# Optimization experiments

Measured on AMD Instinct MI355X. Metric: run time of the kernel, lower is better.

The kernel has to match this reference:

```python
import jax, jax.numpy as jnp
import numpy as np
from jax import lax

B, C, H, W = 8, 512, 48, 48
E = 512          # embed_dim (== in_channels, required by GLoR fusion channel math)
P = 128          # ContextBlock planes = int(512*0.25)
NC = 2           # num_classes; also used (buggily, but faithfully) as BGAM threshold
TOPK_RATIO = 0.1


def conv1x1(x, w, b=None):
    # w: [out, in]
    y = jnp.einsum('bchw,oc->bohw', x, w)
    if b is not None:
        y = y + b[None, :, None, None]
    return y


def conv3x3(x, w, b):
    y = lax.conv_general_dilated(x, w, (1, 1), 'SAME',
                                 dimension_numbers=('NCHW', 'OIHW', 'NCHW'))
    return y + b[None, :, None, None]


def dwconv3x3(x, w):
    # depthwise: w [C,1,3,3], feature_group_count=C
    return lax.conv_general_dilated(x, w, (1, 1), 'SAME',
                                    dimension_numbers=('NCHW', 'OIHW', 'NCHW'),
                                    feature_group_count=x.shape[1])


def bn_eval(x, g, b):
    # eval-mode BatchNorm2d, running_mean=0, running_var=1, eps=1e-5
    scale = g / jnp.sqrt(1.0 + 1e-5)
    return x * scale[None, :, None, None] + b[None, :, None, None]


def chan_mlp(c, w1, b1, g, bl, w2, b2):
    # ContextBlock channel transform: 1x1 conv -> LayerNorm([P,1,1]) -> ReLU -> 1x1 conv, on [B,C] vectors
    h = c @ w1.T + b1                                  # [B,P]
    mu = h.mean(-1, keepdims=True)
    var = jnp.var(h, axis=-1, keepdims=True)
    h = (h - mu) / jnp.sqrt(var + 1e-5) * g + bl
    h = jax.nn.relu(h)
    return h @ w2.T + b2                               # [B,C]


def cos_self(t):
    # torch F.cosine_similarity(t, t, dim=1): dot/(max(n,eps)*max(n,eps)), eps=1e-8
    nrm2 = jnp.sum(t * t, axis=1)                      # [B,H,W]
    n = jnp.maximum(jnp.sqrt(nrm2), 1e-8)
    return nrm2 / (n * n)


def setup_inputs() -> dict:
    key = jax.random.key(0)
    ks = iter(jax.random.split(key, 64))
    def nrm(shape, scale):
        return (jax.random.normal(next(ks), shape) * scale).astype(jnp.float32)
    def gma(n):
        return (1.0 + 0.05 * jax.random.normal(next(ks), (n,))).astype(jnp.float32)
    def bta(n):
        return (0.05 * jax.random.normal(next(ks), (n,))).astype(jnp.float32)
    sC = 1.0 / np.sqrt(C)
    return dict(
        x=jax.random.normal(next(ks), (B, C, H, W), jnp.float32),
        # GLoR local ConvBranch
        lb_w1=nrm((E, C), sC), lb_g1=gma(E), lb_b1=bta(E),
        lb_w2=nrm((E, 1, 3, 3), 1.0 / 3.0), lb_g2=gma(E), lb_b2=bta(E),
        lb_w3=nrm((E, E), 1.0 / np.sqrt(E)), lb_g3=gma(E), lb_b3=bta(E),
        # GLoR ContextBlock (att pooling, channel_add + channel_mul)
        cm_w=nrm((1, C), sC), cm_b=bta(1),
        ca_w1=nrm((P, C), sC), ca_b1=bta(P), ca_lg=gma(P), ca_lb=bta(P),
        ca_w2=nrm((C, P), 1.0 / np.sqrt(P)), ca_b2=bta(C),
        cmu_w1=nrm((P, C), sC), cmu_b1=bta(P), cmu_lg=gma(P), cmu_lb=bta(P),
        cmu_w2=nrm((C, P), 1.0 / np.sqrt(P)), cmu_b2=bta(C),
        fu_w=nrm((E, 2 * E), 1.0 / np.sqrt(2 * E)), fu_b=bta(E),
        # heads
        sh_w=nrm((NC, E), 1.0 / np.sqrt(E)), sh_b=bta(NC),
        bh_w=nrm((2, E), 1.0 / np.sqrt(E)), bh_b=bta(2),
        # ReverseAttention
        ra_w1=nrm((2, 2, 3, 3), 1.0 / np.sqrt(18)), ra_b1=bta(2), ra_g1=gma(2), ra_bb1=bta(2),
        ra_w2=nrm((2, 2, 3, 3), 1.0 / np.sqrt(18)), ra_b2=bta(2), ra_g2=gma(2), ra_bb2=bta(2),
        # AGCR (all bias=False)
        q_w=nrm((E // 4, E), 1.0 / np.sqrt(E)), k_w=nrm((E // 4, E), 1.0 / np.sqrt(E)),
        v_w=nrm((E, E), 1.0 / np.sqrt(E)), fin_w=nrm((E, 2 * E), 1.0 / np.sqrt(2 * E)),
    )


def reference(x, lb_w1, lb_g1, lb_b1, lb_w2, lb_g2, lb_b2, lb_w3, lb_g3, lb_b3,
              cm_w, cm_b, ca_w1, ca_b1, ca_lg, ca_lb, ca_w2, ca_b2,
              cmu_w1, cmu_b1, cmu_lg, cmu_lb, cmu_w2, cmu_b2, fu_w, fu_b,
              sh_w, sh_b, bh_w, bh_b,
              ra_w1, ra_b1, ra_g1, ra_bb1, ra_w2, ra_b2, ra_g2, ra_bb2,
              q_w, k_w, v_w, fin_w):
    b_, c_, h_, w_ = x.shape
    N = h_ * w_
    # ---- GLoR: local ConvBranch ----
    t = jax.nn.relu(bn_eval(conv1x1(x, lb_w1), lb_g1, lb_b1))
    t = jax.nn.relu(bn_eval(dwconv3x3(t, lb_w2), lb_g2, lb_b2))
    local = bn_eval(conv1x1(t, lb_w3), lb_g3, lb_b3)
    # ---- GLoR: ContextBlock (att pooling) ----
    xf = x.reshape(b_, c_, N)
    mask = (conv1x1(x, cm_w, cm_b)).reshape(b_, 1, N)
    mask = jax.nn.softmax(mask, axis=2)
    ctx = jnp.einsum('bcn,bn->bc', xf, mask[:, 0, :])              # [B,C]
    mul = jax.nn.sigmoid(chan_mlp(ctx, cmu_w1, cmu_b1, cmu_lg, cmu_lb, cmu_w2, cmu_b2))
    add = chan_mlp(ctx, ca_w1, ca_b1, ca_lg, ca_lb, ca_w2, ca_b2)
    glob = x * mul[:, :, None, None] + add[:, :, None, None]
    gx = conv1x1(jnp.concatenate([local, glob], axis=1), fu_w, fu_b)  # [B,E,H,W]
    # ---- heads ----
    sem = conv1x1(gx, sh_w, sh_b)                                   # [B,NC,H,W]
    bdl = conv1x1(gx, bh_w, bh_b)                                   # [B,2,H,W]
    # ---- ReverseAttention(boundary_logits, sigmoid(boundary_logits)) ----
    wx = bdl * (1.0 - jax.nn.sigmoid(bdl))
    r = jax.nn.relu(bn_eval(conv3x3(wx, ra_w1, ra_b1), ra_g1, ra_bb1))
    r = jax.nn.relu(bn_eval(conv3x3(r, ra_w2, ra_b2), ra_g2, ra_bb2))
    # ---- BGAM (threshold = num_classes, faithful to source) ----
    thr = jnp.float32(NC)
    st = (cos_self(sem) > thr).astype(x.dtype)
    bt = (cos_self(r) > thr).astype(x.dtype)
    region = ((1.0 - st) * (1.0 - bt))[:, None]                     # [B,1,H,W]
    # ---- AGCR custom attention ----
    k_num = int(N * TOPK_RATIO)
    q = conv1x1(gx, q_w).reshape(b_, -1, N)                         # [B,E/4,N]
    kk = conv1x1(gx, k_w).reshape(b_, -1, N)
    v = conv1x1(gx, v_w).reshape(b_, E, N)
    attn = jnp.einsum('bdm,bdn->bmn', q, kk) / jnp.sqrt(jnp.float32(q.shape[1]))
    aw = jax.nn.softmax(attn, axis=-1)                              # [B,N,N]
    topv, _ = lax.top_k(aw, k_num)
    soft = topv.mean(-1)                                            # [B,N]
    aw = aw * soft[:, None, :]
    # bmm(value, aw^T).mean(-1) == value @ aw.mean(rows)
    col_mean = aw.mean(axis=1)                                      # [B,N]
    ctx2 = jnp.einsum('bcn,bn->bc', v, col_mean)                    # [B,E]
    ctx2 = jnp.broadcast_to(ctx2[:, :, None, None], gx.shape)
    refined = jnp.concatenate([gx, ctx2 * region], axis=1)          # [B,2E,H,W]
    return conv1x1(refined, fin_w)                                  # [B,E,H,W]
```

## Files before the change

### kernel.cpp

```cpp
#include <hip/hip_runtime.h>
#include <math.h>

#define NPIX 2304
#define NCH  512
#define NB   8
#define KNUM 230

typedef unsigned short u16;
typedef __attribute__((ext_vector_type(8))) short short8v;
typedef __attribute__((ext_vector_type(4))) float float4v;

__device__ __forceinline__ float bf2f(u16 u) {
    union { unsigned v; float f; } x; x.v = ((unsigned)u) << 16; return x.f;
}
__device__ __forceinline__ u16 f2bf(float f) {
    union { float f; unsigned v; } x; x.f = f;
    unsigned r = x.v + 0x7FFFu + ((x.v >> 16) & 1u);
    return (u16)(r >> 16);
}

__device__ __forceinline__ float waveSum(float v) {
    #pragma unroll
    for (int o = 32; o > 0; o >>= 1) v += __shfl_down(v, o);
    return v;
}
__device__ __forceinline__ float blockSum256(float v, float* sc4) {
    v = waveSum(v);
    __syncthreads();
    if ((threadIdx.x & 63) == 0) sc4[threadIdx.x >> 6] = v;
    __syncthreads();
    return sc4[0] + sc4[1] + sc4[2] + sc4[3];
}
__device__ __forceinline__ float waveMaxF(float v) {
    #pragma unroll
    for (int o = 32; o > 0; o >>= 1) v = fmaxf(v, __shfl_down(v, o));
    return v;
}
__device__ __forceinline__ float blockMax256(float v, float* sc4) {
    v = waveMaxF(v);
    __syncthreads();
    if ((threadIdx.x & 63) == 0) sc4[threadIdx.x >> 6] = v;
    __syncthreads();
    return fmaxf(fmaxf(sc4[0], sc4[1]), fmaxf(sc4[2], sc4[3]));
}

__device__ __forceinline__ void gl_lds16(const u16* g, u16* l) {
    __builtin_amdgcn_global_load_lds(
        reinterpret_cast<const unsigned __attribute__((address_space(1)))*>(
            reinterpret_cast<uintptr_t>(g)),
        reinterpret_cast<unsigned __attribute__((address_space(3)))*>(
            reinterpret_cast<uintptr_t>(l)),
        16, 0, 0);
}

__global__ __launch_bounds__(256, 3) void mfma_gemm(
    const u16* __restrict__ A, int ldA, long sA,
    const u16* __restrict__ B0, const u16* __restrict__ B1, int ldB, long sB,
    void* __restrict__ outp, int ldO, long sO,
    const float* __restrict__ scaleR, const float* __restrict__ biasR,
    const float* __restrict__ biasC, int ldbc,
    int K, float alpha, int flags)
{
    __shared__ u16 lA[128 * 64];
    __shared__ u16 lB[128 * 64];
    const int t  = threadIdx.x;
    const int w  = t >> 6, l = t & 63;
    const int wR = w >> 1, wC = w & 1;
    const int lg = l >> 4, lr = l & 15, l7 = l & 7;
    const int b   = blockIdx.z;
    const int Cl0 = blockIdx.x * 128;
    const int R0  = blockIdx.y * 128;
    const u16* Ab  = A + (size_t)b * sA;
    const u16* B0b = B0 + (size_t)b * sB;
    const u16* B1b = B1 ? B1 + (size_t)b * sB : nullptr;

    float4v acc[4][4];
    const float4v zero = {0.f, 0.f, 0.f, 0.f};
    #pragma unroll
    for (int i = 0; i < 4; ++i)
        #pragma unroll
        for (int j = 0; j < 4; ++j) acc[i][j] = zero;

    const int sr = t >> 3;
    const int sp = t & 7;

    for (int k0 = 0; k0 < K; k0 += 64) {
        const u16* Bsrc = B0b; int kb = k0;
        if (B1b && k0 >= 512) { Bsrc = B1b; kb = k0 - 512; }
        #pragma unroll
        for (int i = 0; i < 4; ++i) {
            const int r  = i * 32 + sr;
            const int ca = sp ^ (r & 7);
            gl_lds16(Ab   + (size_t)(R0  + r) * ldA + (k0 + ca * 8), &lA[i * 2048 + t * 8]);
            gl_lds16(Bsrc + (size_t)(Cl0 + r) * ldB + (kb + ca * 8), &lB[i * 2048 + t * 8]);
        }
        __syncthreads();
        #pragma unroll
        for (int kk = 0; kk < 2; ++kk) {
            short8v af[4], bfv[4];
            const int p = (kk * 4 + lg) ^ l7;
            #pragma unroll
            for (int mt = 0; mt < 4; ++mt) {
                const int rA = wR * 64 + mt * 16 + lr;
                af[mt]  = *reinterpret_cast<const short8v*>(&lA[rA * 64 + p * 8]);
                const int rB = wC * 64 + mt * 16 + lr;
                bfv[mt] = *reinterpret_cast<const short8v*>(&lB[rB * 64 + p * 8]);
            }
            #pragma unroll
            for (int mt = 0; mt < 4; ++mt)
                #pragma unroll
                for (int nt = 0; nt < 4; ++nt)
                    acc[mt][nt] = __builtin_amdgcn_mfma_f32_16x16x32_bf16(
                        af[mt], bfv[nt], acc[mt][nt], 0, 0, 0);
        }
        __syncthreads();
    }

    const bool relu = (flags & 1), f32o = (flags & 2);
    #pragma unroll
    for (int nt = 0; nt < 4; ++nt) {
        const int Cl = Cl0 + wC * 64 + nt * 16 + lr;
        const float bc = biasC ? biasC[(size_t)b * ldbc + Cl] : 0.f;
        #pragma unroll
        for (int mt = 0; mt < 4; ++mt) {
            const int Rb = R0 + wR * 64 + mt * 16 + lg * 4;
            float4 scv = scaleR ? *reinterpret_cast<const float4*>(&scaleR[Rb])
                                : make_float4(1.f, 1.f, 1.f, 1.f);
            float4 bv  = biasR  ? *reinterpret_cast<const float4*>(&biasR[Rb])
                                : make_float4(0.f, 0.f, 0.f, 0.f);
            float vals[4];
            #pragma unroll
            for (int j = 0; j < 4; ++j) {
                const float sc = alpha * ((&scv.x)[j]);
                float v = acc[mt][nt][j] * sc + (&bv.x)[j] + bc;
                if (relu) v = fmaxf(v, 0.f);
                vals[j] = v;
            }
            if (f32o) {
                float* op = (float*)outp + (size_t)b * sO + (size_t)Cl * ldO + Rb;
                *reinterpret_cast<float4*>(op) = make_float4(vals[0], vals[1], vals[2], vals[3]);
            } else {
                ushort4 u;
                u.x = f2bf(vals[0]); u.y = f2bf(vals[1]);
                u.z = f2bf(vals[2]); u.w = f2bf(vals[3]);
                u16* op = (u16*)outp + (size_t)b * sO + (size_t)Cl * ldO + Rb;
                *reinterpret_cast<ushort4*>(op) = u;
            }
        }
    }
}

__global__ __launch_bounds__(256) void transpose_cvt(
    const float* __restrict__ x, u16* __restrict__ xb)
{
    __shared__ float tile[64][65];
    const int t = threadIdx.x;
    const int n0 = blockIdx.x * 64, c0 = blockIdx.y * 64, b = blockIdx.z;
    const int tr = t >> 4, tc4 = (t & 15) * 4;
    #pragma unroll
    for (int i = 0; i < 4; ++i) {
        const int cc = tr + i * 16;
        float4 v = *reinterpret_cast<const float4*>(
            x + ((size_t)(b * NCH + c0 + cc)) * NPIX + n0 + tc4);
        tile[cc][tc4 + 0] = v.x; tile[cc][tc4 + 1] = v.y;
        tile[cc][tc4 + 2] = v.z; tile[cc][tc4 + 3] = v.w;
    }
    __syncthreads();
    #pragma unroll
    for (int i = 0; i < 4; ++i) {
        const int nn = tr + i * 16;
        ushort4 u;
        u.x = f2bf(tile[tc4 + 0][nn]); u.y = f2bf(tile[tc4 + 1][nn]);
        u.z = f2bf(tile[tc4 + 2][nn]); u.w = f2bf(tile[tc4 + 3][nn]);
        *reinterpret_cast<ushort4*>(xb + ((size_t)b * NPIX + n0 + nn) * NCH + c0 + tc4) = u;
    }
}

__global__ __launch_bounds__(256) void cvt_bf16(
    const float* __restrict__ s, u16* __restrict__ d, int n4)
{
    const int i = blockIdx.x * 256 + threadIdx.x;
    if (i < n4) {
        float4 v = reinterpret_cast<const float4*>(s)[i];
        ushort4 u; u.x = f2bf(v.x); u.y = f2bf(v.y); u.z = f2bf(v.z); u.w = f2bf(v.w);
        reinterpret_cast<ushort4*>(d)[i] = u;
    }
}

__global__ __launch_bounds__(256) void fold_dw(
    const float* __restrict__ wsrc, const float* __restrict__ g, float* __restrict__ wf)
{
    const int i = blockIdx.x * 256 + threadIdx.x;
    if (i < 9 * NCH) {
        const int c = i / 9, tap = i % 9;
        wf[tap * NCH + c] = wsrc[i] * g[c] * 0.99999500003749978f;
    }
}

__global__ __launch_bounds__(256) void dwconv_k(
    const u16* __restrict__ t1, const float* __restrict__ wf,
    const float* __restrict__ b2, u16* __restrict__ t2)
{
    const int idx = blockIdx.x * 256 + threadIdx.x;
    const int cq = idx & 127;
    const int n  = (idx >> 7) % NPIX;
    const int b  = (idx >> 7) / NPIX;
    const int c  = cq * 4;
    const int y = n / 48, x = n % 48;
    float s0 = 0.f, s1 = 0.f, s2 = 0.f, s3 = 0.f;
    #pragma unroll
    for (int dy = -1; dy <= 1; ++dy) {
        const int yy = y + dy;
        if (yy < 0 || yy >= 48) continue;
        #pragma unroll
        for (int dx = -1; dx <= 1; ++dx) {
            const int xx = x + dx;
            if (xx < 0 || xx >= 48) continue;
            ushort4 tv = *reinterpret_cast<const ushort4*>(
                &t1[((size_t)b * NPIX + yy * 48 + xx) * NCH + c]);
            float4 wv = *reinterpret_cast<const float4*>(
                &wf[((dy + 1) * 3 + dx + 1) * NCH + c]);
            s0 = fmaf(bf2f(tv.x), wv.x, s0); s1 = fmaf(bf2f(tv.y), wv.y, s1);
            s2 = fmaf(bf2f(tv.z), wv.z, s2); s3 = fmaf(bf2f(tv.w), wv.w, s3);
        }
    }
    float4 bb = *reinterpret_cast<const float4*>(&b2[c]);
    ushort4 o;
    o.x = f2bf(fmaxf(s0 + bb.x, 0.f)); o.y = f2bf(fmaxf(s1 + bb.y, 0.f));
    o.z = f2bf(fmaxf(s2 + bb.z, 0.f)); o.w = f2bf(fmaxf(s3 + bb.w, 0.f));
    *reinterpret_cast<ushort4*>(&t2[((size_t)b * NPIX + n) * NCH + c]) = o;
}

__global__ __launch_bounds__(256) void mask_logits_k(
    const u16* __restrict__ xb, const float* __restrict__ cmw,
    const float* __restrict__ cmb, float* __restrict__ logits)
{
    const int w = threadIdx.x >> 6, l = threadIdx.x & 63;
    const int n = blockIdx.x * 4 + w, b = blockIdx.y;
    const ushort4* row = reinterpret_cast<const ushort4*>(xb + ((size_t)b * NPIX + n) * NCH);
    const int c0 = l * 8;
    ushort4 u0 = row[l * 2], u1 = row[l * 2 + 1];
    float4 w0 = *reinterpret_cast<const float4*>(&cmw[c0]);
    float4 w1 = *reinterpret_cast<const float4*>(&cmw[c0 + 4]);
    float s = bf2f(u0.x) * w0.x + bf2f(u0.y) * w0.y + bf2f(u0.z) * w0.z + bf2f(u0.w) * w0.w
            + bf2f(u1.x) * w1.x + bf2f(u1.y) * w1.y + bf2f(u1.z) * w1.z + bf2f(u1.w) * w1.w;
    s = waveSum(s);
    if (l == 0) logits[(size_t)b * NPIX + n] = s + cmb[0];
}

__global__ __launch_bounds__(256) void softmax_mask(
    const float* __restrict__ logits, float* __restrict__ mask)
{
    __shared__ float sc[4];
    const int b = blockIdx.x, t = threadIdx.x;
    const float* lr = logits + (size_t)b * NPIX;
    float mx = -3.4e38f;
    for (int i = t; i < NPIX; i += 256) mx = fmaxf(mx, lr[i]);
    mx = blockMax256(mx, sc);
    float s = 0.f;
    for (int i = t; i < NPIX; i += 256) s += __expf(lr[i] - mx);
    s = blockSum256(s, sc);
    const float inv = 1.0f / s;
    for (int i = t; i < NPIX; i += 256) mask[(size_t)b * NPIX + i] = __expf(lr[i] - mx) * inv;
}

__global__ __launch_bounds__(512) void ctx_pool_k(
    const u16* __restrict__ xb, const float* __restrict__ mask, float* __restrict__ ctx)
{
    const int c = threadIdx.x, b = blockIdx.y;
    const int nn0 = blockIdx.x * 128;
    float s = 0.f;
    for (int n = nn0; n < nn0 + 128; ++n)
        s = fmaf(bf2f(xb[((size_t)b * NPIX + n) * NCH + c]), mask[(size_t)b * NPIX + n], s);
    atomicAdd(&ctx[b * NCH + c], s);
}

__global__ __launch_bounds__(256) void chan_h(
    const float* __restrict__ ctxv,
    const float* __restrict__ mw1, const float* __restrict__ mb1,
    const float* __restrict__ aw1, const float* __restrict__ ab1,
    float* __restrict__ hnb)
{
    const int w = threadIdx.x >> 6, l = threadIdx.x & 63;
    const int gid = blockIdx.x * 4 + w;
    const int path = gid >> 10;
    const int rem  = gid & 1023;
    const int h = rem >> 3, b = rem & 7;
    const float* W1 = path ? aw1 : mw1;
    const float* B1 = path ? ab1 : mb1;
    const float4 wa = *reinterpret_cast<const float4*>(&W1[h * 512 + l * 8]);
    const float4 wb = *reinterpret_cast<const float4*>(&W1[h * 512 + l * 8 + 4]);
    const float4 ca = *reinterpret_cast<const float4*>(&ctxv[b * 512 + l * 8]);
    const float4 cb = *reinterpret_cast<const float4*>(&ctxv[b * 512 + l * 8 + 4]);
    float s = wa.x * ca.x + wa.y * ca.y + wa.z * ca.z + wa.w * ca.w
            + wb.x * cb.x + wb.y * cb.y + wb.z * cb.z + wb.w * cb.w;
    s = waveSum(s);
    if (l == 0) hnb[(path * 8 + b) * 128 + h] = s + B1[h];
}

__global__ __launch_bounds__(128) void chan_ln(
    const float* __restrict__ mlg, const float* __restrict__ mlb,
    const float* __restrict__ alg, const float* __restrict__ alb,
    float* __restrict__ hnb)
{
    __shared__ float sc[2];
    const int path = blockIdx.x, b = blockIdx.y, t = threadIdx.x;
    float* hp = hnb + (path * 8 + b) * 128;
    const float v = hp[t];
    float s1 = waveSum(v);
    if ((t & 63) == 0) sc[t >> 6] = s1;
    __syncthreads();
    const float mu = (sc[0] + sc[1]) * (1.0f / 128.0f);
    const float d = v - mu;
    float s2 = waveSum(d * d);
    __syncthreads();
    if ((t & 63) == 0) sc[t >> 6] = s2;
    __syncthreads();
    const float var = (sc[0] + sc[1]) * (1.0f / 128.0f);
    const float* LG = path ? alg : mlg;
    const float* LB = path ? alb : mlb;
    hp[t] = fmaxf(d / sqrtf(var + 1e-5f) * LG[t] + LB[t], 0.f);
}

__global__ __launch_bounds__(128) void chan_o(
    const float* __restrict__ hnb,
    const float* __restrict__ mw2, const float* __restrict__ mb2,
    const float* __restrict__ aw2, const float* __restrict__ ab2,
    float* __restrict__ mulo, float* __restrict__ addo)
{
    __shared__ float hs[128];
    const int oc = blockIdx.x, path = blockIdx.y, b = blockIdx.z;
    const int t = threadIdx.x;
    hs[t] = hnb[(path * 8 + b) * 128 + t];
    __syncthreads();
    const int o = oc * 128 + t;
    const float* W2 = path ? aw2 : mw2;
    float s = (path ? ab2 : mb2)[o];
    #pragma unroll
    for (int p = 0; p < 128; p += 4) {
        const float4 wv = *reinterpret_cast<const float4*>(&W2[o * 128 + p]);
        s += wv.x * hs[p] + wv.y * hs[p + 1] + wv.z * hs[p + 2] + wv.w * hs[p + 3];
    }
    if (path == 0) mulo[b * 512 + o] = 1.0f / (1.0f + __expf(-s));
    else           addo[b * 512 + o] = s;
}

__global__ __launch_bounds__(256) void glob_ew_k(
    const u16* __restrict__ xb, const float* __restrict__ mulv,
    const float* __restrict__ addv, u16* __restrict__ g)
{
    const int idx = blockIdx.x * 256 + threadIdx.x;
    const int cq = idx & 63;
    const int n = (idx >> 6) % NPIX;
    const int b = (idx >> 6) / NPIX;
    const int c = cq * 8;
    const size_t base = ((size_t)b * NPIX + n) * NCH + c;
    ushort4 u0 = *reinterpret_cast<const ushort4*>(&xb[base]);
    ushort4 u1 = *reinterpret_cast<const ushort4*>(&xb[base + 4]);
    const float* mp = &mulv[b * NCH + c];
    const float* ap = &addv[b * NCH + c];
    float4 m0 = *reinterpret_cast<const float4*>(mp);
    float4 m1 = *reinterpret_cast<const float4*>(mp + 4);
    float4 a0 = *reinterpret_cast<const float4*>(ap);
    float4 a1 = *reinterpret_cast<const float4*>(ap + 4);
    ushort4 o0, o1;
    o0.x = f2bf(fmaf(bf2f(u0.x), m0.x, a0.x));
    o0.y = f2bf(fmaf(bf2f(u0.y), m0.y, a0.y));
    o0.z = f2bf(fmaf(bf2f(u0.z), m0.z, a0.z));
    o0.w = f2bf(fmaf(bf2f(u0.w), m0.w, a0.w));
    o1.x = f2bf(fmaf(bf2f(u1.x), m1.x, a1.x));
    o1.y = f2bf(fmaf(bf2f(u1.y), m1.y, a1.y));
    o1.z = f2bf(fmaf(bf2f(u1.z), m1.z, a1.z));
    o1.w = f2bf(fmaf(bf2f(u1.w), m1.w, a1.w));
    *reinterpret_cast<ushort4*>(&g[base]) = o0;
    *reinterpret_cast<ushort4*>(&g[base + 4]) = o1;
}

__global__ __launch_bounds__(256) void softmax_topk_wave(
    const u16* __restrict__ p, float* __restrict__ mxo,
    float* __restrict__ invSo, float* __restrict__ softo, int bOff)
{
    const int w = threadIdx.x >> 6, l = threadIdx.x & 63;
    const int r = blockIdx.x * 4 + w;
    const int bc = blockIdx.y;
    const u16* pr = p + ((size_t)bc * NPIX + r) * NPIX;
    const uint4* p16 = reinterpret_cast<const uint4*>(pr);
    uint4 q0 = p16[l], q1 = p16[64 + l], q2 = p16[128 + l], q3 = p16[192 + l];
    uint2 q4 = reinterpret_cast<const uint2*>(pr)[512 + l];
    unsigned uw[18] = {q0.x, q0.y, q0.z, q0.w, q1.x, q1.y, q1.z, q1.w,
                       q2.x, q2.y, q2.z, q2.w, q3.x, q3.y, q3.z, q3.w,
                       q4.x, q4.y};
    unsigned km[36];
    #pragma unroll
    for (int i = 0; i < 18; ++i) {
        const unsigned v = uw[i];
        const unsigned m = ((v >> 15) & 0x10001u) * 0x7FFFu + 0x80008000u;
        const unsigned s = v ^ m;
        km[2 * i]     = s & 0xFFFFu;
        km[2 * i + 1] = s >> 16;
    }
    unsigned kmax = km[0];
    #pragma unroll
    for (int i = 1; i < 36; ++i) kmax = max(kmax, km[i]);
    #pragma unroll
    for (int o = 32; o > 0; o >>= 1) kmax = max(kmax, (unsigned)__shfl_xor((int)kmax, o));
    const unsigned mxbits = (kmax & 0x8000u) ? (kmax ^ 0x8000u) : (kmax ^ 0xFFFFu);
    const float mx = bf2f((u16)mxbits);
    unsigned kt = 0u;
    for (int bit = 15; bit >= 0; --bit) {
        const unsigned cand = kt | (1u << bit);
        int c = 0;
        #pragma unroll
        for (int i = 0; i < 36; ++i)
            c += (int)__popcll(__ballot(km[i] >= cand));
        if (c >= KNUM) kt = cand;
    }
    const unsigned tbits = (kt & 0x8000u) ? (kt ^ 0x8000u) : (kt ^ 0xFFFFu);
    const float te = __expf(bf2f((u16)tbits) - mx);
    float S = 0.f, ss = 0.f; int a = 0;
    #pragma unroll
    for (int i = 0; i < 36; ++i) {
        const unsigned bb = (km[i] & 0x8000u) ? (km[i] ^ 0x8000u) : (km[i] ^ 0xFFFFu);
        const float e = __expf(bf2f((u16)bb) - mx);
        S += e;
        const bool gt = km[i] > kt;
        if (gt) ss += e;
        a += (int)__popcll(__ballot(gt));
    }
    #pragma unroll
    for (int o = 32; o > 0; o >>= 1) { S += __shfl_xor(S, o); ss += __shfl_xor(ss, o); }
    if (l == 0) {
        const size_t gi = (size_t)(bOff + bc) * NPIX + r;
        mxo[gi] = mx; invSo[gi] = 1.0f / S;
        softo[gi] = (ss + (float)(KNUM - a) * te) / (S * (float)KNUM);
    }
}

__global__ __launch_bounds__(256) void colsum_k(
    const u16* __restrict__ p, const float* __restrict__ mxo,
    const float* __restrict__ invSo, float* __restrict__ colsum, int bOff)
{
    const int j = blockIdx.x * 256 + threadIdx.x;
    const int ic0 = blockIdx.y * 72;
    const int bc = blockIdx.z;
    const float* mxr = mxo + (size_t)(bOff + bc) * NPIX;
    const float* isr = invSo + (size_t)(bOff + bc) * NPIX;
    const u16* pb = p + (size_t)bc * NPIX * NPIX;
    float s = 0.f;
    #pragma unroll 4
    for (int i = ic0; i < ic0 + 72; ++i)
        s += __expf(bf2f(pb[(size_t)i * NPIX + j]) - mxr[i]) * isr[i];
    atomicAdd(&colsum[(size_t)(bOff + bc) * NPIX + j], s);
}

__global__ __launch_bounds__(512) void ctx2_pool_k(
    const u16* __restrict__ qkv, const float* __restrict__ colsum,
    const float* __restrict__ soft, float* __restrict__ ctx2)
{
    const int c = threadIdx.x, b = blockIdx.y;
    const int nn0 = blockIdx.x * 128;
    float s = 0.f;
    for (int n = nn0; n < nn0 + 128; ++n) {
        const float wgt = colsum[(size_t)b * NPIX + n] * soft[(size_t)b * NPIX + n];
        s = fmaf(bf2f(qkv[((size_t)b * NPIX + n) * 768 + 256 + c]), wgt, s);
    }
    atomicAdd(&ctx2[b * NCH + c], s * (1.0f / (float)NPIX));
}

__global__ __launch_bounds__(256) void compute_z(
    const float* __restrict__ finw, const float* __restrict__ ctx2, float* __restrict__ z)
{
    const int o = blockIdx.x * 256 + threadIdx.x;
    const int b = blockIdx.y;
    const float* c2 = ctx2 + b * NCH;
    const float* wr = finw + (size_t)o * 1024 + 512;
    float s = 0.f;
    for (int c = 0; c < NCH; ++c) s = fmaf(wr[c], c2[c], s);
    z[b * NCH + o] = s;
}

extern "C" void kernel_launch(void* const* d_in, const int* in_sizes, int n_in,
                              void* d_out, int out_size, void* d_ws, size_t ws_size,
                              hipStream_t stream)
{
    (void)in_sizes; (void)n_in; (void)out_size; (void)ws_size;
    const float* x      = (const float*)d_in[0];
    const float* lb_w1  = (const float*)d_in[1];
    const float* lb_g1  = (const float*)d_in[2];
    const float* lb_b1  = (const float*)d_in[3];
    const float* lb_w2  = (const float*)d_in[4];
    const float* lb_g2  = (const float*)d_in[5];
    const float* lb_b2  = (const float*)d_in[6];
    const float* lb_w3  = (const float*)d_in[7];
    const float* lb_g3  = (const float*)d_in[8];
    const float* lb_b3  = (const float*)d_in[9];
    const float* cm_w   = (const float*)d_in[10];
    const float* cm_b   = (const float*)d_in[11];
    const float* ca_w1  = (const float*)d_in[12];
    const float* ca_b1  = (const float*)d_in[13];
    const float* ca_lg  = (const float*)d_in[14];
    const float* ca_lb  = (const float*)d_in[15];
    const float* ca_w2  = (const float*)d_in[16];
    const float* ca_b2  = (const float*)d_in[17];
    const float* cmu_w1 = (const float*)d_in[18];
    const float* cmu_b1 = (const float*)d_in[19];
    const float* cmu_lg = (const float*)d_in[20];
    const float* cmu_lb = (const float*)d_in[21];
    const float* cmu_w2 = (const float*)d_in[22];
    const float* cmu_b2 = (const float*)d_in[23];
    const float* fu_w   = (const float*)d_in[24];
    const float* fu_b   = (const float*)d_in[25];
    const float* q_w    = (const float*)d_in[38];
    const float* k_w    = (const float*)d_in[39];
    const float* v_w    = (const float*)d_in[40];
    const float* fin_w  = (const float*)d_in[41];

    char* W = (char*)d_ws;
    const size_t SZ_ACT = (size_t)NB * NPIX * NCH * 2;
    u16* xb   = (u16*)(W);
    u16* bufA = (u16*)(W + SZ_ACT);
    u16* bufB = (u16*)(W + 2 * SZ_ACT);
    u16* gx   = (u16*)(W + 3 * SZ_ACT);
    u16* qkv  = (u16*)(W + 4 * SZ_ACT);
    char* SM = W + 4 * SZ_ACT + (size_t)NB * NPIX * 768 * 2;
    float* logits = (float*)SM; SM += (size_t)NB * NPIX * 4;
    float* maskb  = (float*)SM; SM += (size_t)NB * NPIX * 4;
    float* mxb    = (float*)SM; SM += (size_t)NB * NPIX * 4;
    float* invSb  = (float*)SM; SM += (size_t)NB * NPIX * 4;
    float* softb  = (float*)SM; SM += (size_t)NB * NPIX * 4;
    float* colsum = (float*)SM; SM += (size_t)NB * NPIX * 4;
    float* ctxb   = (float*)SM; SM += (size_t)NB * NCH * 4;
    float* ctx2b  = (float*)SM; SM += (size_t)NB * NCH * 4;
    float* mulb   = (float*)SM; SM += (size_t)NB * NCH * 4;
    float* addb   = (float*)SM; SM += (size_t)NB * NCH * 4;
    float* zbuf   = (float*)SM; SM += (size_t)NB * NCH * 4;
    float* hnb    = (float*)SM; SM += (size_t)2 * NB * 128 * 4;
    float* wfold  = (float*)SM; SM += (size_t)9 * NCH * 4;
    u16* w1b   = (u16*)SM; SM += (size_t)512 * 512 * 2;
    u16* w3b   = (u16*)SM; SM += (size_t)512 * 512 * 2;
    u16* fuwb  = (u16*)SM; SM += (size_t)512 * 1024 * 2;
    u16* finwb = (u16*)SM; SM += (size_t)512 * 1024 * 2;
    u16* qkvwb = (u16*)SM; SM += (size_t)768 * 512 * 2;
    u16* pbuf = xb;

    const float invs  = 0.99999500003749978f;
    const float rs128 = 0.08838834764831845f;
    const long SACT = (long)NPIX * NCH;

    cvt_bf16<<<256, 256, 0, stream>>>(lb_w1, w1b, 65536);
    cvt_bf16<<<256, 256, 0, stream>>>(lb_w3, w3b, 65536);
    cvt_bf16<<<512, 256, 0, stream>>>(fu_w, fuwb, 131072);
    cvt_bf16<<<512, 256, 0, stream>>>(fin_w, finwb, 131072);
    cvt_bf16<<<64, 256, 0, stream>>>(q_w, qkvwb, 16384);
    cvt_bf16<<<64, 256, 0, stream>>>(k_w, qkvwb + 128 * 512, 16384);
    cvt_bf16<<<256, 256, 0, stream>>>(v_w, qkvwb + 256 * 512, 65536);
    fold_dw<<<18, 256, 0, stream>>>(lb_w2, lb_g2, wfold);
    transpose_cvt<<<dim3(36, 8, 8), 256, 0, stream>>>(x, xb);
    hipMemsetAsync(colsum, 0, (size_t)NB * NPIX * 4 + 2 * (size_t)NB * NCH * 4, stream);

    mfma_gemm<<<dim3(18, 4, 8), 256, 0, stream>>>(w1b, 512, 0, xb, nullptr, 512, SACT,
        bufA, 512, SACT, lb_g1, lb_b1, nullptr, 0, 512, invs, 1);
    dwconv_k<<<9216, 256, 0, stream>>>(bufA, wfold, lb_b2, bufB);
    mfma_gemm<<<dim3(18, 4, 8), 256, 0, stream>>>(w3b, 512, 0, bufB, nullptr, 512, SACT,
        bufA, 512, SACT, lb_g3, lb_b3, nullptr, 0, 512, invs, 0);
    mask_logits_k<<<dim3(576, 8), 256, 0, stream>>>(xb, cm_w, cm_b, logits);
    softmax_mask<<<8, 256, 0, stream>>>(logits, maskb);
    ctx_pool_k<<<dim3(18, 8), 512, 0, stream>>>(xb, maskb, ctxb);
    chan_h<<<512, 256, 0, stream>>>(ctxb, cmu_w1, cmu_b1, ca_w1, ca_b1, hnb);
    chan_ln<<<dim3(2, 8), 128, 0, stream>>>(cmu_lg, cmu_lb, ca_lg, ca_lb, hnb);
    chan_o<<<dim3(4, 2, 8), 128, 0, stream>>>(hnb, cmu_w2, cmu_b2, ca_w2, ca_b2, mulb, addb);
    glob_ew_k<<<4608, 256, 0, stream>>>(xb, mulb, addb, bufB);
    mfma_gemm<<<dim3(18, 4, 8), 256, 0, stream>>>(fuwb, 1024, 0, bufA, bufB, 512, SACT,
        gx, 512, SACT, nullptr, fu_b, nullptr, 0, 1024, 1.0f, 0);
    mfma_gemm<<<dim3(18, 6, 8), 256, 0, stream>>>(qkvwb, 512, 0, gx, nullptr, 512, SACT,
        qkv, 768, (long)NPIX * 768, nullptr, nullptr, nullptr, 0, 512, 1.0f, 0);
    for (int cc = 0; cc < 2; ++cc) {
        const u16* kp = qkv + (size_t)cc * 4 * NPIX * 768 + 128;
        const u16* qp = qkv + (size_t)cc * 4 * NPIX * 768;
        mfma_gemm<<<dim3(18, 18, 4), 256, 0, stream>>>(kp, 768, (long)NPIX * 768,
            qp, nullptr, 768, (long)NPIX * 768,
            pbuf, NPIX, (long)NPIX * NPIX, nullptr, nullptr, nullptr, 0, 128, rs128, 0);
        softmax_topk_wave<<<dim3(576, 4), 256, 0, stream>>>(pbuf, mxb, invSb, softb, cc * 4);
        colsum_k<<<dim3(9, 32, 4), 256, 0, stream>>>(pbuf, mxb, invSb, colsum, cc * 4);
    }
    ctx2_pool_k<<<dim3(18, 8), 512, 0, stream>>>(qkv, colsum, softb, ctx2b);
    compute_z<<<dim3(2, 8), 256, 0, stream>>>(fin_w, ctx2b, zbuf);
    mfma_gemm<<<dim3(4, 18, 8), 256, 0, stream>>>(gx, 512, SACT, finwb, nullptr, 1024, 0,
        d_out, NPIX, (long)NCH * NPIX, nullptr, nullptr, zbuf, 512, 512, 1.0f, 2);
}
```

Measured before the change: 382.1 us.

## Fold conv3 and global scaling into fusion weights; fuse colsum into softmax

The fusion 1x1 conv weights are pre-multiplied with the BN-scaled conv3 weights and, per batch, with the ContextBlock channel multiplier. This removes the separate conv3 GEMM and the elementwise glob kernel, and a per-batch row bias carries the folded bias terms. The attention column sums are now accumulated inside the softmax/top-k kernel through LDS atomics, so the separate colsum pass that re-read the NxN matrix is gone. The cost is extra weight-prep GEMM work, per-batch weight copies, and changed bf16 rounding order.

```diff
diff --git a/kernel.cpp b/kernel.cpp
--- a/kernel.cpp
+++ b/kernel.cpp
@@ -59,6 +59,7 @@
     void* __restrict__ outp, int ldO, long sO,
     const float* __restrict__ scaleR, const float* __restrict__ biasR,
     const float* __restrict__ biasC, int ldbc,
+    const float* __restrict__ biasRB, int ldrb,
     int K, float alpha, int flags)
 {
     __shared__ u16 lA[128 * 64];
@@ -128,11 +129,13 @@
                                 : make_float4(1.f, 1.f, 1.f, 1.f);
             float4 bv  = biasR  ? *reinterpret_cast<const float4*>(&biasR[Rb])
                                 : make_float4(0.f, 0.f, 0.f, 0.f);
+            float4 rbv = biasRB ? *reinterpret_cast<const float4*>(&biasRB[(size_t)b * ldrb + Rb])
+                                : make_float4(0.f, 0.f, 0.f, 0.f);
             float vals[4];
             #pragma unroll
             for (int j = 0; j < 4; ++j) {
                 const float sc = alpha * ((&scv.x)[j]);
-                float v = acc[mt][nt][j] * sc + (&bv.x)[j] + bc;
+                float v = acc[mt][nt][j] * sc + (&bv.x)[j] + bc + (&rbv.x)[j];
                 if (relu) v = fmaxf(v, 0.f);
                 vals[j] = v;
             }
@@ -173,6 +176,32 @@
         u.x = f2bf(tile[tc4 + 0][nn]); u.y = f2bf(tile[tc4 + 1][nn]);
         u.z = f2bf(tile[tc4 + 2][nn]); u.w = f2bf(tile[tc4 + 3][nn]);
         *reinterpret_cast<ushort4*>(xb + ((size_t)b * NPIX + n0 + nn) * NCH + c0 + tc4) = u;
+    }
+}
+
+__global__ __launch_bounds__(256) void transpose_w3(
+    const float* __restrict__ w3, const float* __restrict__ g3, u16* __restrict__ w3t)
+{
+    __shared__ float tile[64][65];
+    const int t = threadIdx.x;
+    const int k0 = blockIdx.x * 64, c0 = blockIdx.y * 64;
+    const int tr = t >> 4, tc4 = (t & 15) * 4;
+    #pragma unroll
+    for (int i = 0; i < 4; ++i) {
+        const int cc = tr + i * 16;
+        const float s = g3[c0 + cc] * 0.99999500003749978f;
+        float4 v = *reinterpret_cast<const float4*>(&w3[(size_t)(c0 + cc) * 512 + k0 + tc4]);
+        tile[cc][tc4 + 0] = v.x * s; tile[cc][tc4 + 1] = v.y * s;
+        tile[cc][tc4 + 2] = v.z * s; tile[cc][tc4 + 3] = v.w * s;
+    }
+    __syncthreads();
+    #pragma unroll
+    for (int i = 0; i < 4; ++i) {
+        const int kk = tr + i * 16;
+        ushort4 u;
+        u.x = f2bf(tile[tc4 + 0][kk]); u.y = f2bf(tile[tc4 + 1][kk]);
+        u.z = f2bf(tile[tc4 + 2][kk]); u.w = f2bf(tile[tc4 + 3][kk]);
+        *reinterpret_cast<ushort4*>(&w3t[(size_t)(k0 + kk) * 512 + c0 + tc4]) = u;
     }
 }
 
@@ -345,44 +374,51 @@
     else           addo[b * 512 + o] = s;
 }
 
-__global__ __launch_bounds__(256) void glob_ew_k(
-    const u16* __restrict__ xb, const float* __restrict__ mulv,
-    const float* __restrict__ addv, u16* __restrict__ g)
+__global__ __launch_bounds__(256) void scale_wglob(
+    const float* __restrict__ fuw, const float* __restrict__ mulv, u16* __restrict__ wf)
 {
     const int idx = blockIdx.x * 256 + threadIdx.x;
-    const int cq = idx & 63;
-    const int n = (idx >> 6) % NPIX;
-    const int b = (idx >> 6) / NPIX;
-    const int c = cq * 8;
-    const size_t base = ((size_t)b * NPIX + n) * NCH + c;
-    ushort4 u0 = *reinterpret_cast<const ushort4*>(&xb[base]);
-    ushort4 u1 = *reinterpret_cast<const ushort4*>(&xb[base + 4]);
-    const float* mp = &mulv[b * NCH + c];
-    const float* ap = &addv[b * NCH + c];
-    float4 m0 = *reinterpret_cast<const float4*>(mp);
-    float4 m1 = *reinterpret_cast<const float4*>(mp + 4);
-    float4 a0 = *reinterpret_cast<const float4*>(ap);
-    float4 a1 = *reinterpret_cast<const float4*>(ap + 4);
-    ushort4 o0, o1;
-    o0.x = f2bf(fmaf(bf2f(u0.x), m0.x, a0.x));
-    o0.y = f2bf(fmaf(bf2f(u0.y), m0.y, a0.y));
-    o0.z = f2bf(fmaf(bf2f(u0.z), m0.z, a0.z));
-    o0.w = f2bf(fmaf(bf2f(u0.w), m0.w, a0.w));
-    o1.x = f2bf(fmaf(bf2f(u1.x), m1.x, a1.x));
-    o1.y = f2bf(fmaf(bf2f(u1.y), m1.y, a1.y));
-    o1.z = f2bf(fmaf(bf2f(u1.z), m1.z, a1.z));
-    o1.w = f2bf(fmaf(bf2f(u1.w), m1.w, a1.w));
-    *reinterpret_cast<ushort4*>(&g[base]) = o0;
-    *reinterpret_cast<ushort4*>(&g[base + 4]) = o1;
+    const int cq = idx & 127;
+    const int o  = (idx >> 7) & 511;
+    const int b  = idx >> 16;
+    const int c  = cq * 4;
+    float4 w = *reinterpret_cast<const float4*>(&fuw[(size_t)o * 1024 + 512 + c]);
+    float4 m = *reinterpret_cast<const float4*>(&mulv[b * 512 + c]);
+    ushort4 u;
+    u.x = f2bf(w.x * m.x); u.y = f2bf(w.y * m.y);
+    u.z = f2bf(w.z * m.z); u.w = f2bf(w.w * m.w);
+    *reinterpret_cast<ushort4*>(&wf[(size_t)b * 524288 + (size_t)o * 1024 + 512 + c]) = u;
+}
+
+__global__ __launch_bounds__(256) void fuse_bias(
+    const float* __restrict__ fuw, const float* __restrict__ fub,
+    const float* __restrict__ b3, const float* __restrict__ addv, float* __restrict__ fb)
+{
+    const int o = blockIdx.x * 256 + threadIdx.x;
+    const int b = blockIdx.y;
+    const float* wr = fuw + (size_t)o * 1024;
+    float s = fub[o];
+    for (int c = 0; c < 512; c += 4) {
+        float4 w1 = *reinterpret_cast<const float4*>(&wr[c]);
+        float4 bv = *reinterpret_cast<const float4*>(&b3[c]);
+        float4 w2 = *reinterpret_cast<const float4*>(&wr[512 + c]);
+        float4 av = *reinterpret_cast<const float4*>(&addv[b * 512 + c]);
+        s += w1.x * bv.x + w1.y * bv.y + w1.z * bv.z + w1.w * bv.w
+           + w2.x * av.x + w2.y * av.y + w2.z * av.z + w2.w * av.w;
+    }
+    fb[b * 512 + o] = s;
 }
 
 __global__ __launch_bounds__(256) void softmax_topk_wave(
-    const u16* __restrict__ p, float* __restrict__ mxo,
-    float* __restrict__ invSo, float* __restrict__ softo, int bOff)
-{
-    const int w = threadIdx.x >> 6, l = threadIdx.x & 63;
+    const u16* __restrict__ p, float* __restrict__ colsum,
+    float* __restrict__ softo, int bOff)
+{
+    __shared__ float cls[NPIX];
+    const int t = threadIdx.x;
+    const int w = t >> 6, l = t & 63;
     const int r = blockIdx.x * 4 + w;
     const int bc = blockIdx.y;
+    for (int i = t; i < NPIX; i += 256) cls[i] = 0.f;
     const u16* pr = p + ((size_t)bc * NPIX + r) * NPIX;
     const uint4* p16 = reinterpret_cast<const uint4*>(pr);
     uint4 q0 = p16[l], q1 = p16[64 + l], q2 = p16[128 + l], q3 = p16[192 + l];
@@ -426,31 +462,29 @@
         const bool gt = km[i] > kt;
         if (gt) ss += e;
         a += (int)__popcll(__ballot(gt));
+        km[i] = __float_as_uint(e);
     }
     #pragma unroll
     for (int o = 32; o > 0; o >>= 1) { S += __shfl_xor(S, o); ss += __shfl_xor(ss, o); }
+    const float invS = 1.0f / S;
     if (l == 0) {
-        const size_t gi = (size_t)(bOff + bc) * NPIX + r;
-        mxo[gi] = mx; invSo[gi] = 1.0f / S;
-        softo[gi] = (ss + (float)(KNUM - a) * te) / (S * (float)KNUM);
-    }
-}
-
-__global__ __launch_bounds__(256) void colsum_k(
-    const u16* __restrict__ p, const float* __restrict__ mxo,
-    const float* __restrict__ invSo, float* __restrict__ colsum, int bOff)
-{
-    const int j = blockIdx.x * 256 + threadIdx.x;
-    const int ic0 = blockIdx.y * 72;
-    const int bc = blockIdx.z;
-    const float* mxr = mxo + (size_t)(bOff + bc) * NPIX;
-    const float* isr = invSo + (size_t)(bOff + bc) * NPIX;
-    const u16* pb = p + (size_t)bc * NPIX * NPIX;
-    float s = 0.f;
-    #pragma unroll 4
-    for (int i = ic0; i < ic0 + 72; ++i)
-        s += __expf(bf2f(pb[(size_t)i * NPIX + j]) - mxr[i]) * isr[i];
-    atomicAdd(&colsum[(size_t)(bOff + bc) * NPIX + j], s);
+        softo[(size_t)(bOff + bc) * NPIX + r] =
+            (ss + (float)(KNUM - a) * te) * invS * (1.0f / (float)KNUM);
+    }
+    __syncthreads();
+    #pragma unroll
+    for (int i = 0; i < 32; ++i) {
+        const int col = 512 * (i >> 3) + 8 * l + (i & 7);
+        atomicAdd(&cls[col], __uint_as_float(km[i]) * invS);
+    }
+    #pragma unroll
+    for (int i = 32; i < 36; ++i) {
+        const int col = 2048 + 4 * l + (i - 32);
+        atomicAdd(&cls[col], __uint_as_float(km[i]) * invS);
+    }
+    __syncthreads();
+    float* cb = colsum + (size_t)(bOff + bc) * NPIX;
+    for (int i = t; i < NPIX; i += 256) atomicAdd(&cb[i], cls[i]);
 }
 
 __global__ __launch_bounds__(512) void ctx2_pool_k(
@@ -522,11 +556,10 @@
     u16* bufB = (u16*)(W + 2 * SZ_ACT);
     u16* gx   = (u16*)(W + 3 * SZ_ACT);
     u16* qkv  = (u16*)(W + 4 * SZ_ACT);
+    u16* wfused = qkv;
     char* SM = W + 4 * SZ_ACT + (size_t)NB * NPIX * 768 * 2;
     float* logits = (float*)SM; SM += (size_t)NB * NPIX * 4;
     float* maskb  = (float*)SM; SM += (size_t)NB * NPIX * 4;
-    float* mxb    = (float*)SM; SM += (size_t)NB * NPIX * 4;
-    float* invSb  = (float*)SM; SM += (size_t)NB * NPIX * 4;
     float* softb  = (float*)SM; SM += (size_t)NB * NPIX * 4;
     float* colsum = (float*)SM; SM += (size_t)NB * NPIX * 4;
     float* ctxb   = (float*)SM; SM += (size_t)NB * NCH * 4;
@@ -534,13 +567,14 @@
     float* mulb   = (float*)SM; SM += (size_t)NB * NCH * 4;
     float* addb   = (float*)SM; SM += (size_t)NB * NCH * 4;
     float* zbuf   = (float*)SM; SM += (size_t)NB * NCH * 4;
+    float* fbias  = (float*)SM; SM += (size_t)NB * NCH * 4;
     float* hnb    = (float*)SM; SM += (size_t)2 * NB * 128 * 4;
     float* wfold  = (float*)SM; SM += (size_t)9 * NCH * 4;
     u16* w1b   = (u16*)SM; SM += (size_t)512 * 512 * 2;
-    u16* w3b   = (u16*)SM; SM += (size_t)512 * 512 * 2;
     u16* fuwb  = (u16*)SM; SM += (size_t)512 * 1024 * 2;
     u16* finwb = (u16*)SM; SM += (size_t)512 * 1024 * 2;
     u16* qkvwb = (u16*)SM; SM += (size_t)768 * 512 * 2;
+    u16* w3t   = (u16*)SM; SM += (size_t)512 * 512 * 2;
     u16* pbuf = xb;
 
     const float invs  = 0.99999500003749978f;
@@ -548,7 +582,6 @@
     const long SACT = (long)NPIX * NCH;
 
     cvt_bf16<<<256, 256, 0, stream>>>(lb_w1, w1b, 65536);
-    cvt_bf16<<<256, 256, 0, stream>>>(lb_w3, w3b, 65536);
     cvt_bf16<<<512, 256, 0, stream>>>(fu_w, fuwb, 131072);
     cvt_bf16<<<512, 256, 0, stream>>>(fin_w, finwb, 131072);
     cvt_bf16<<<64, 256, 0, stream>>>(q_w, qkvwb, 16384);
@@ -556,35 +589,39 @@
     cvt_bf16<<<256, 256, 0, stream>>>(v_w, qkvwb + 256 * 512, 65536);
     fold_dw<<<18, 256, 0, stream>>>(lb_w2, lb_g2, wfold);
     transpose_cvt<<<dim3(36, 8, 8), 256, 0, stream>>>(x, xb);
+    transpose_w3<<<dim3(8, 8), 256, 0, stream>>>(lb_w3, lb_g3, w3t);
     hipMemsetAsync(colsum, 0, (size_t)NB * NPIX * 4 + 2 * (size_t)NB * NCH * 4, stream);
 
+    mfma_gemm<<<dim3(4, 4, 8), 256, 0, stream>>>(w3t, 512, 0, fuwb, nullptr, 1024, 0,
+        wfused, 1024, 524288, nullptr, nullptr, nullptr, 0, nullptr, 0, 512, 1.0f, 0);
+
     mfma_gemm<<<dim3(18, 4, 8), 256, 0, stream>>>(w1b, 512, 0, xb, nullptr, 512, SACT,
-        bufA, 512, SACT, lb_g1, lb_b1, nullptr, 0, 512, invs, 1);
+        bufA, 512, SACT, lb_g1, lb_b1, nullptr, 0, nullptr, 0, 512, invs, 1);
     dwconv_k<<<9216, 256, 0, stream>>>(bufA, wfold, lb_b2, bufB);
-    mfma_gemm<<<dim3(18, 4, 8), 256, 0, stream>>>(w3b, 512, 0, bufB, nullptr, 512, SACT,
-        bufA, 512, SACT, lb_g3, lb_b3, nullptr, 0, 512, invs, 0);
     mask_logits_k<<<dim3(576, 8), 256, 0, stream>>>(xb, cm_w, cm_b, logits);
     softmax_mask<<<8, 256, 0, stream>>>(logits, maskb);
     ctx_pool_k<<<dim3(18, 8), 512, 0, stream>>>(xb, maskb, ctxb);
     chan_h<<<512, 256, 0, stream>>>(ctxb, cmu_w1, cmu_b1, ca_w1, ca_b1, hnb);
     chan_ln<<<dim3(2, 8), 128, 0, stream>>>(cmu_lg, cmu_lb, ca_lg, ca_lb, hnb);
     chan_o<<<dim3(4, 2, 8), 128, 0, stream>>>(hnb, cmu_w2, cmu_b2, ca_w2, ca_b2, mulb, addb);
-    glob_ew_k<<<4608, 256, 0, stream>>>(xb, mulb, addb, bufB);
-    mfma_gemm<<<dim3(18, 4, 8), 256, 0, stream>>>(fuwb, 1024, 0, bufA, bufB, 512, SACT,
-        gx, 512, SACT, nullptr, fu_b, nullptr, 0, 1024, 1.0f, 0);
+    scale_wglob<<<2048, 256, 0, stream>>>(fu_w, mulb, wfused);
+    fuse_bias<<<dim3(2, 8), 256, 0, stream>>>(fu_w, fu_b, lb_b3, addb, fbias);
+    mfma_gemm<<<dim3(18, 4, 8), 256, 0, stream>>>(wfused, 1024, 524288, bufB, xb, 512, SACT,
+        gx, 512, SACT, nullptr, nullptr, nullptr, 0, fbias, 512, 1024, 1.0f, 0);
     mfma_gemm<<<dim3(18, 6, 8), 256, 0, stream>>>(qkvwb, 512, 0, gx, nullptr, 512, SACT,
-        qkv, 768, (long)NPIX * 768, nullptr, nullptr, nullptr, 0, 512, 1.0f, 0);
+        qkv, 768, (long)NPIX * 768, nullptr, nullptr, nullptr, 0, nullptr, 0, 512, 1.0f, 0);
     for (int cc = 0; cc < 2; ++cc) {
         const u16* kp = qkv + (size_t)cc * 4 * NPIX * 768 + 128;
         const u16* qp = qkv + (size_t)cc * 4 * NPIX * 768;
         mfma_gemm<<<dim3(18, 18, 4), 256, 0, stream>>>(kp, 768, (long)NPIX * 768,
             qp, nullptr, 768, (long)NPIX * 768,
-            pbuf, NPIX, (long)NPIX * NPIX, nullptr, nullptr, nullptr, 0, 128, rs128, 0);
-        softmax_topk_wave<<<dim3(576, 4), 256, 0, stream>>>(pbuf, mxb, invSb, softb, cc * 4);
-        colsum_k<<<dim3(9, 32, 4), 256, 0, stream>>>(pbuf, mxb, invSb, colsum, cc * 4);
+            pbuf, NPIX, (long)NPIX * NPIX, nullptr, nullptr, nullptr, 0, nullptr, 0,
+            128, rs128, 0);
+        softmax_topk_wave<<<dim3(576, 4), 256, 0, stream>>>(pbuf, colsum, softb, cc * 4);
     }
     ctx2_pool_k<<<dim3(18, 8), 512, 0, stream>>>(qkv, colsum, softb, ctx2b);
     compute_z<<<dim3(2, 8), 256, 0, stream>>>(fin_w, ctx2b, zbuf);
     mfma_gemm<<<dim3(4, 18, 8), 256, 0, stream>>>(gx, 512, SACT, finwb, nullptr, 1024, 0,
-        d_out, NPIX, (long)NCH * NPIX, nullptr, nullptr, zbuf, 512, 512, 1.0f, 2);
-}
+        d_out, NPIX, (long)NCH * NPIX, nullptr, nullptr, zbuf, 512, nullptr, 0,
+        512, 1.0f, 2);
+}
```

After: 600.0 us. 1.57x slower.
